# Optimization experiments

Hardware: AMD Instinct MI355X
Metric: run time of the kernel (lower is better)

Reference implementation:

```python
import jax, jax.numpy as jnp
import numpy as np

NUM_MODALS = 4
SHARED_IDX = 3  # forward always uses adapter index 3 as the shared LoRA

def setup_inputs() -> dict:
    key = jax.random.key(0)
    k1, k2, k3, k4, k5 = jax.random.split(key, 5)
    M, B, n, c, r = NUM_MODALS, 8, 1024, 768, 16
    x = jax.random.normal(k1, (M * B, n, c), dtype=jnp.float32)
    Wp = jax.random.normal(k2, (c, c), dtype=jnp.float32) * 0.02   # proj weight [out,in]
    bp = jax.random.normal(k3, (c,), dtype=jnp.float32) * 0.02     # proj bias
    A = jax.random.normal(k4, (M, r, c), dtype=jnp.float32) * 0.02  # linear_a_o weights [r,c]
    Bw = jax.random.normal(k5, (M, c, r), dtype=jnp.float32) * 0.02 # linear_b_o weights [c,r]
    return {"x": x, "Wp": Wp, "bp": bp, "A": A, "Bw": Bw}

def reference(x, Wp, bp, A, Bw):
    bs_m, n, c = x.shape
    xm = x.reshape(NUM_MODALS, -1, n, c)  # [M,B,n,c]
    # base projection (dense GEMM) + bias
    base = jnp.einsum('mbnc,oc->mbno', xm, Wp) + bp
    # shared LoRA (adapter index 3 for every modality)
    sh_lo = jnp.einsum('mbnc,rc->mbnr', xm, A[SHARED_IDX])
    shared = jnp.einsum('mbnr,or->mbno', sh_lo, Bw[SHARED_IDX])
    # modality-specific LoRA (batched over modality axis)
    sp_lo = jnp.einsum('mbnc,mrc->mbnr', xm, A)
    specific = jnp.einsum('mbnr,mor->mbno', sp_lo, Bw)
    out = base + shared + specific
    return out.reshape(bs_m, n, -1)
```

## Files before the change

kernel.cpp:

```cpp
#include <hip/hip_runtime.h>
#include <hip/hip_bf16.h>
#include <stdint.h>

#define NUM_MODALS 4
#define SHARED_IDX 3

typedef __attribute__((ext_vector_type(8))) short bf16x8;
typedef __attribute__((ext_vector_type(4))) float floatx4;

__device__ __forceinline__ unsigned short f2bf(float f) {
  unsigned int u = __float_as_uint(f);
  u += 0x7fffu + ((u >> 16) & 1u);
  return (unsigned short)(u >> 16);
}

__global__ __launch_bounds__(256) void weff_fast(
    const float* __restrict__ Wp, const float* __restrict__ A,
    const float* __restrict__ Bw, unsigned short* __restrict__ Weff) {
  const int c  = blockIdx.x * 256 + threadIdx.x;
  const int o0 = blockIdx.y * 16;
  const int m  = blockIdx.z;

  __shared__ float b3[256], bm[256];
  const int t = threadIdx.x;
  {
    const int o = o0 + (t >> 4);
    const int r = t & 15;
    b3[t] = Bw[(SHARED_IDX * 768 + o) * 16 + r];
    bm[t] = Bw[((size_t)m * 768 + o) * 16 + r];
  }
  __syncthreads();

  float a3[16], am[16];
#pragma unroll
  for (int r = 0; r < 16; ++r) {
    a3[r] = A[(SHARED_IDX * 16 + r) * 768 + c];
    am[r] = A[((size_t)m * 16 + r) * 768 + c];
  }
#pragma unroll 4
  for (int oo = 0; oo < 16; ++oo) {
    const int o = o0 + oo;
    float acc = Wp[(size_t)o * 768 + c];
#pragma unroll
    for (int r = 0; r < 16; ++r) {
      acc += b3[oo * 16 + r] * a3[r];
      acc += bm[oo * 16 + r] * am[r];
    }
    Weff[((size_t)m * 768 + o) * 768 + c] = f2bf(acc);
  }
}

__global__ __launch_bounds__(256) void lora_gemm_fused(
    const float* __restrict__ X,
    const unsigned short* __restrict__ Weff,
    const float* __restrict__ bp,
    float* __restrict__ out) {
  const int bid = blockIdx.x;
  const int xcd = bid & 7;
  const int s   = bid >> 3;
  const int w   = xcd * 192 + s;
  const int ct  = w % 6;
  const int rt  = w / 6;
  const int m        = rt >> 6;
  const int row_base = (rt & 63) * 128;
  const int col_base = ct * 128;

  __shared__ alignas(16) unsigned short As[128 * 64];
  __shared__ alignas(16) unsigned short Ws[128 * 64];

  const int tid  = threadIdx.x;
  const int wave = tid >> 6;
  const int lane = tid & 63;
  const int ln = lane & 15;
  const int qd = lane >> 4;
  const int wm = wave & 1;
  const int wn = wave >> 1;

  const float*          Xm = X    + (size_t)m * 8192 * 768;
  const unsigned short* Wm = Weff + (size_t)m * 768 * 768;

  floatx4 acc[4][4];
#pragma unroll
  for (int i = 0; i < 4; ++i)
#pragma unroll
    for (int j = 0; j < 4; ++j)
      acc[i][j] = (floatx4)(0.0f);

  const int xr   = tid >> 4;
  const int xc   = (tid & 15) * 4;
  const int cb   = xc >> 3;
  const int half = (xc >> 2) & 1;
  const float* xsrc[8];
  unsigned short* xdst[8];
#pragma unroll
  for (int p = 0; p < 8; ++p) {
    const int r = xr + p * 16;
    xsrc[p] = Xm + (size_t)(row_base + r) * 768 + xc;
    xdst[p] = &As[r * 64 + (cb ^ (r & 7)) * 8 + half * 4];
  }
  const int sr = lane >> 3;
  const int ss = lane & 7;
  const unsigned short* wsrc[4];
#pragma unroll
  for (int p = 0; p < 4; ++p) {
    const int r = wave * 32 + p * 8 + sr;
    wsrc[p] = Wm + (size_t)(col_base + r) * 768 + (ss ^ (r & 7)) * 8;
  }

  for (int kt = 0; kt < 12; ++kt) {
#pragma unroll
    for (int p = 0; p < 4; ++p) {
      __builtin_amdgcn_global_load_lds(
          (const __attribute__((address_space(1))) void*)wsrc[p],
          (__attribute__((address_space(3))) void*)&Ws[(wave * 32 + p * 8) * 64],
          16, 0, 0);
      wsrc[p] += 64;
    }
#pragma unroll
    for (int p = 0; p < 8; ++p) {
      const float4 v = *(const float4*)xsrc[p];
      xsrc[p] += 64;
      __hip_bfloat162 h0 = __float22bfloat162_rn(make_float2(v.x, v.y));
      __hip_bfloat162 h1 = __float22bfloat162_rn(make_float2(v.z, v.w));
      uint2 hv;
      hv.x = *(unsigned int*)&h0;
      hv.y = *(unsigned int*)&h1;
      *(uint2*)xdst[p] = hv;
    }
    __syncthreads();

#pragma unroll
    for (int kk = 0; kk < 64; kk += 32) {
      const int kblk = (kk >> 3) + qd;
      const int slot = (kblk ^ (ln & 7)) * 8;
      bf16x8 a[4], b[4];
#pragma unroll
      for (int i = 0; i < 4; ++i)
        a[i] = *(const bf16x8*)(&As[(wm * 64 + i * 16 + ln) * 64 + slot]);
#pragma unroll
      for (int j = 0; j < 4; ++j)
        b[j] = *(const bf16x8*)(&Ws[(wn * 64 + j * 16 + ln) * 64 + slot]);
#pragma unroll
      for (int i = 0; i < 4; ++i)
#pragma unroll
        for (int j = 0; j < 4; ++j)
          acc[i][j] = __builtin_amdgcn_mfma_f32_16x16x32_bf16(a[i], b[j], acc[i][j], 0, 0, 0);
    }
    __syncthreads();
  }

  float* Om = out + (size_t)m * 8192 * 768;
#pragma unroll
  for (int j = 0; j < 4; ++j) {
    const int o = col_base + wn * 64 + j * 16 + ln;
    const float bias = bp[o];
#pragma unroll
    for (int i = 0; i < 4; ++i) {
      const int R = row_base + wm * 64 + i * 16 + qd * 4;
      float* dst = Om + (size_t)R * 768 + o;
#pragma unroll
      for (int v = 0; v < 4; ++v)
        dst[(size_t)v * 768] = acc[i][j][v] + bias;
    }
  }
}

extern "C" void kernel_launch(void* const* d_in, const int* in_sizes, int n_in,
                              void* d_out, int out_size, void* d_ws, size_t ws_size,
                              hipStream_t stream) {
  const float* x  = (const float*)d_in[0];
  const float* Wp = (const float*)d_in[1];
  const float* bp = (const float*)d_in[2];
  const float* A  = (const float*)d_in[3];
  const float* Bw = (const float*)d_in[4];
  float* out = (float*)d_out;

  unsigned short* Weff = (unsigned short*)d_ws;

  weff_fast<<<dim3(3, 48, 4), 256, 0, stream>>>(Wp, A, Bw, Weff);
  lora_gemm_fused<<<dim3(1536), 256, 0, stream>>>(x, Weff, bp, out);
}
```

Measured before the change: 241.7 us.

## Double-buffer LDS tiles and register-prefetch X in fused LoRA GEMM

Adds a two-stage pipeline to the main GEMM loop. The next K-tile of X is loaded into registers and the next W tile is loaded asynchronously into a second LDS buffer while the current tile's MFMAs run. This also drops the trailing barrier per iteration, aiming to hide global-load latency behind compute. The cost is doubled LDS use (64 KB per block), which can lower occupancy, plus extra registers for the prefetched X values.

New measurement: 241.7 us. No clear change (+0.0%).

```diff
diff --git a/kernel.cpp b/kernel.cpp
--- a/kernel.cpp
+++ b/kernel.cpp
@@ -65,8 +65,8 @@
   const int row_base = (rt & 63) * 128;
   const int col_base = ct * 128;
 
-  __shared__ alignas(16) unsigned short As[128 * 64];
-  __shared__ alignas(16) unsigned short Ws[128 * 64];
+  __shared__ alignas(16) unsigned short As[2 * 128 * 64];
+  __shared__ alignas(16) unsigned short Ws[2 * 128 * 64];
 
   const int tid  = threadIdx.x;
   const int wave = tid >> 6;
@@ -107,27 +107,54 @@
     wsrc[p] = Wm + (size_t)(col_base + r) * 768 + (ss ^ (r & 7)) * 8;
   }
 
+  float4 xv[8];
+#pragma unroll
+  for (int p = 0; p < 8; ++p) {
+    xv[p] = *(const float4*)xsrc[p];
+    xsrc[p] += 64;
+  }
+#pragma unroll
+  for (int p = 0; p < 4; ++p) {
+    __builtin_amdgcn_global_load_lds(
+        (const __attribute__((address_space(1))) void*)wsrc[p],
+        (__attribute__((address_space(3))) void*)&Ws[(wave * 32 + p * 8) * 64],
+        16, 0, 0);
+    wsrc[p] += 64;
+  }
+
   for (int kt = 0; kt < 12; ++kt) {
-#pragma unroll
-    for (int p = 0; p < 4; ++p) {
-      __builtin_amdgcn_global_load_lds(
-          (const __attribute__((address_space(1))) void*)wsrc[p],
-          (__attribute__((address_space(3))) void*)&Ws[(wave * 32 + p * 8) * 64],
-          16, 0, 0);
-      wsrc[p] += 64;
-    }
+    const int boff = (kt & 1) * (128 * 64);
+
 #pragma unroll
     for (int p = 0; p < 8; ++p) {
-      const float4 v = *(const float4*)xsrc[p];
-      xsrc[p] += 64;
+      const float4 v = xv[p];
       __hip_bfloat162 h0 = __float22bfloat162_rn(make_float2(v.x, v.y));
       __hip_bfloat162 h1 = __float22bfloat162_rn(make_float2(v.z, v.w));
       uint2 hv;
       hv.x = *(unsigned int*)&h0;
       hv.y = *(unsigned int*)&h1;
-      *(uint2*)xdst[p] = hv;
-    }
+      *(uint2*)(xdst[p] + boff) = hv;
+    }
+
     __syncthreads();
+
+    if (kt < 11) {
+      const int nboff = boff ^ (128 * 64);
+#pragma unroll
+      for (int p = 0; p < 8; ++p) {
+        xv[p] = *(const float4*)xsrc[p];
+        xsrc[p] += 64;
+      }
+#pragma unroll
+      for (int p = 0; p < 4; ++p) {
+        __builtin_amdgcn_global_load_lds(
+            (const __attribute__((address_space(1))) void*)wsrc[p],
+            (__attribute__((address_space(3))) void*)&Ws[nboff + (wave * 32 + p * 8) * 64],
+            16, 0, 0);
+        wsrc[p] += 64;
+      }
+      __builtin_amdgcn_sched_barrier(0);
+    }
 
 #pragma unroll
     for (int kk = 0; kk < 64; kk += 32) {
@@ -136,17 +163,16 @@
       bf16x8 a[4], b[4];
 #pragma unroll
       for (int i = 0; i < 4; ++i)
-        a[i] = *(const bf16x8*)(&As[(wm * 64 + i * 16 + ln) * 64 + slot]);
+        a[i] = *(const bf16x8*)(&As[boff + (wm * 64 + i * 16 + ln) * 64 + slot]);
 #pragma unroll
       for (int j = 0; j < 4; ++j)
-        b[j] = *(const bf16x8*)(&Ws[(wn * 64 + j * 16 + ln) * 64 + slot]);
+        b[j] = *(const bf16x8*)(&Ws[boff + (wn * 64 + j * 16 + ln) * 64 + slot]);
 #pragma unroll
       for (int i = 0; i < 4; ++i)
 #pragma unroll
         for (int j = 0; j < 4; ++j)
           acc[i][j] = __builtin_amdgcn_mfma_f32_16x16x32_bf16(a[i], b[j], acc[i][j], 0, 0, 0);
     }
-    __syncthreads();
   }
 
   float* Om = out + (size_t)m * 8192 * 768;
```
